# Performance work log

Hardware: AMD Instinct MI355X
Metric: run time of the kernel (lower is better)

## Reference

```python
import math
import jax, jax.numpy as jnp
import numpy as np

DMODEL = 512
NUM_HEADS = 8
HEAD_DIM = DMODEL // NUM_HEADS
MAX_LEN = 1024
L = 2 * MAX_LEN - 1  # 2047
B = 4
S = 1024  # src_len == max_len


def setup_inputs() -> dict:
    key = jax.random.key(0)
    ks = jax.random.split(key, 12)
    f32 = jnp.float32
    inp = {
        "query": jax.random.normal(ks[0], (B, S, DMODEL), f32),
        "key": jax.random.normal(ks[1], (B, S, DMODEL), f32),
        "value": jax.random.normal(ks[2], (B, S, DMODEL), f32),
        # nn.Linear weights (y = x @ W.T + b)
        "Wq": jax.random.normal(ks[3], (DMODEL, DMODEL), f32) * 0.02,
        "bq": jnp.zeros((DMODEL,), f32),
        "Wk": jax.random.normal(ks[4], (DMODEL, DMODEL), f32) * 0.02,
        "bk": jnp.zeros((DMODEL,), f32),
        "Wv": jax.random.normal(ks[5], (DMODEL, DMODEL), f32) * 0.02,
        "bv": jnp.zeros((DMODEL,), f32),
        # relative position tables (torch.randn init)
        "quaver_Er": jax.random.normal(ks[6], (NUM_HEADS, L, HEAD_DIM), f32),
        "beat_Er": jax.random.normal(ks[7], (NUM_HEADS, L // 4, HEAD_DIM), f32),
        "bar_Er": jax.random.normal(ks[8], (NUM_HEADS, L // 16, HEAD_DIM), f32),
    }
    return inp


def _skew(QEr):
    # QEr: [b, h, S, 2S-1] -> [b, h, S, S] via pad-reshape-slice trick
    b, h, s, l = QEr.shape
    x = jnp.pad(QEr, ((0, 0), (0, 0), (0, 0), (0, 1)))        # [b,h,S,2S]
    x = x.reshape(b, h, -1)                                    # [b,h,S*2S]
    x = jnp.pad(x, ((0, 0), (0, 0), (0, l - s)))               # [b,h,(S+1)*(2S-1)]
    x = x.reshape(b, h, s + 1, l)
    return x[:, :, :s, -s:]


def _skew_chunked(QEr, rep):
    # Faithful to skew_beat/skew_bar: repeat_interleave(rep) along last dim, then
    # roll each chunk of `rep` rows (chunk i) by i*rep, then take last S cols.
    b, h, s, lr = QEr.shape
    x = jnp.repeat(QEr, rep, axis=-1)                          # [b,h,S,rep*lr]
    w = rep * lr
    shifts = (jnp.arange(s) // rep) * rep                      # [S]
    # torch.roll: out[c] = in[(c - shift) mod W]
    cols = (jnp.arange(w)[None, :] - shifts[:, None]) % w      # [S, W]
    x = jnp.take_along_axis(x, cols[None, None], axis=-1)
    return x[:, :, :s, -s:]


def reference(query, key, value, Wq, bq, Wk, bk, Wv, bv, quaver_Er, beat_Er, bar_Er):
    bs, src_len, d_model = query.shape
    h, hd = NUM_HEADS, HEAD_DIM
    max_len = MAX_LEN

    q = (query @ Wq.T + bq).reshape(bs, src_len, h, hd).transpose(0, 2, 1, 3)   # [b,h,S,d]
    k = (key @ Wk.T + bk).reshape(bs, src_len, h, hd).transpose(0, 2, 3, 1)      # [b,h,d,S]
    v = (value @ Wv.T + bv).reshape(bs, src_len, h, hd).transpose(0, 2, 1, 3)    # [b,h,S,d]

    Er_q = quaver_Er[:, max_len - src_len:max_len + src_len, :]                  # [h,2S-1,d]
    Er_b = beat_Er[:, (max_len - src_len) // 4:(max_len + src_len) // 4, :]      # [h,~S/2,d]
    Er_r = bar_Er[:, (max_len - src_len) // 16:(max_len + src_len) // 16, :]     # [h,~S/8,d]

    QEr_q = jnp.einsum('bhsd,hld->bhsl', q, Er_q)
    QEr_b = jnp.einsum('bhsd,hld->bhsl', q, Er_b)
    QEr_r = jnp.einsum('bhsd,hld->bhsl', q, Er_r)

    Srel = _skew(QEr_q)
    Srel_beat = _skew_chunked(QEr_b, 4)
    Srel_bar = _skew_chunked(QEr_r, 16)

    attn = (jnp.matmul(q, k) + Srel + Srel_beat + Srel_bar) / math.sqrt(hd)
    attn = jax.nn.softmax(attn, axis=-1)
    out = jnp.matmul(attn, v)                                                    # [b,h,S,d]
    out = out.transpose(0, 2, 1, 3).reshape(bs, src_len, d_model)
    return out, attn
```

## Files before the change

kernel.cpp:

```cpp
#include <hip/hip_runtime.h>


typedef float f32x4 __attribute__((ext_vector_type(4)));
typedef short s16x8 __attribute__((ext_vector_type(8)));
typedef short s16x4 __attribute__((ext_vector_type(4)));
typedef __bf16 bf16x8 __attribute__((ext_vector_type(8)));

static __device__ __forceinline__ short f2bf(float f) {
    return __builtin_bit_cast(short, (__bf16)f);
}
static __device__ __forceinline__ float bf2f(short s) {
    union { unsigned u; float f; } v;
    v.u = ((unsigned)(unsigned short)s) << 16;
    return v.f;
}
static __device__ __forceinline__ f32x4 MM(s16x8 a, s16x8 b, f32x4 c) {
    return __builtin_amdgcn_mfma_f32_16x16x32_bf16(
        __builtin_bit_cast(bf16x8, a), __builtin_bit_cast(bf16x8, b), c, 0, 0, 0);
}
#define KEEP(x) asm volatile("" : "+v"(x))

struct CvtArgs {
    const float* src[9];
    short* dst[9];
    unsigned n[9];
};

__global__ __launch_bounds__(256) void convert_kernel(CvtArgs a) {
    const int ai = blockIdx.y;
    const unsigned n = a.n[ai];
    const float* __restrict__ s = a.src[ai];
    short* __restrict__ d = a.dst[ai];
    const unsigned stride = gridDim.x * 256 * 8;
    for (unsigned base = (blockIdx.x * 256 + threadIdx.x) * 8; base < n; base += stride) {
        f32x4 v0 = *(const f32x4*)(s + base);
        f32x4 v1 = *(const f32x4*)(s + base + 4);
        s16x8 o;
        o[0] = f2bf(v0[0]); o[1] = f2bf(v0[1]); o[2] = f2bf(v0[2]); o[3] = f2bf(v0[3]);
        o[4] = f2bf(v1[0]); o[5] = f2bf(v1[1]); o[6] = f2bf(v1[2]); o[7] = f2bf(v1[3]);
        *(s16x8*)(d + base) = o;
    }
}

__global__ __launch_bounds__(128, 2) void proj_kernel(
    const short* __restrict__ queryb, const short* __restrict__ keyb, const short* __restrict__ valueb,
    const short* __restrict__ Wqb, const float* __restrict__ bq,
    const short* __restrict__ Wkb, const float* __restrict__ bk,
    const short* __restrict__ Wvb, const float* __restrict__ bv,
    short* __restrict__ qb, short* __restrict__ kb, short* __restrict__ vT)
{
    const int tid = threadIdx.x;
    const int wid = tid >> 6, lane = tid & 63;
    const int l15 = lane & 15, grp = lane >> 4;
    const int gid = blockIdx.x * 2 + wid;
    const int z = gid >> 9;
    const int r = gid & 511;

    const short *Am, *Bm;
    const float* bias;
    int a0, b0;
    if (z == 0)      { Am = Wqb;    Bm = queryb; bias = bq; a0 = (r >> 6) * 64; b0 = (r & 63) * 64; }
    else if (z == 1) { Am = Wkb;    Bm = keyb;   bias = bk; a0 = (r >> 6) * 64; b0 = (r & 63) * 64; }
    else             { Am = valueb; Bm = Wvb;    bias = bv; a0 = (r >> 3) * 64; b0 = (r & 7) * 64; }

    f32x4 acc[4][4];
    #pragma unroll
    for (int i = 0; i < 4; ++i)
        #pragma unroll
        for (int j = 0; j < 4; ++j)
            acc[i][j] = f32x4{0.f, 0.f, 0.f, 0.f};

    const short* arow0 = Am + (size_t)(a0 + l15) * 512 + grp * 8;
    const short* brow0 = Bm + (size_t)(b0 + l15) * 512 + grp * 8;

    s16x8 aA[4], bA[4], aB[4], bB[4];
    #pragma unroll
    for (int i = 0; i < 4; ++i) {
        aA[i] = *(const s16x8*)(arow0 + (size_t)i * 16 * 512);
        bA[i] = *(const s16x8*)(brow0 + (size_t)i * 16 * 512);
    }
    for (int kk = 0; kk < 512; kk += 32) {
        const int kn = kk + 32;
        if (kn < 512) {
            #pragma unroll
            for (int i = 0; i < 4; ++i) {
                aB[i] = *(const s16x8*)(arow0 + (size_t)i * 16 * 512 + kn);
                bB[i] = *(const s16x8*)(brow0 + (size_t)i * 16 * 512 + kn);
            }
        }
        #pragma unroll
        for (int i = 0; i < 4; ++i)
            #pragma unroll
            for (int j = 0; j < 4; ++j)
                acc[i][j] = MM(aA[i], bA[j], acc[i][j]);
        #pragma unroll
        for (int i = 0; i < 4; ++i) { aA[i] = aB[i]; bA[i] = bB[i]; }
    }

    if (z < 2) {
        short* dst = (z == 0) ? qb : kb;
        #pragma unroll
        for (int i = 0; i < 4; ++i) {
            const int f0 = a0 + i * 16 + grp * 4;
            const f32x4 bv4 = *(const f32x4*)&bias[f0];
            const int h = f0 >> 6, d0 = f0 & 63;
            #pragma unroll
            for (int j = 0; j < 4; ++j) {
                const int srow = b0 + j * 16 + l15;
                const int bb = srow >> 10, sl = srow & 1023;
                s16x4 o;
                #pragma unroll
                for (int g = 0; g < 4; ++g)
                    o[g] = f2bf(acc[i][j][g] + bv4[g]);
                *(s16x4*)&dst[(size_t)((bb * 8 + h) * 1024 + sl) * 64 + d0] = o;
            }
        }
    } else {
        #pragma unroll
        for (int j = 0; j < 4; ++j) {
            const int n = b0 + j * 16 + l15;
            const float bval = bias[n];
            const int h = n >> 6, d = n & 63;
            #pragma unroll
            for (int i = 0; i < 4; ++i) {
                const int s0 = a0 + i * 16 + grp * 4;
                const int bb = s0 >> 10, sl = s0 & 1023;
                s16x4 o;
                #pragma unroll
                for (int g = 0; g < 4; ++g)
                    o[g] = f2bf(acc[i][j][g] + bval);
                *(s16x4*)&vT[(size_t)((bb * 8 + h) * 64 + d) * 1024 + sl] = o;
            }
        }
    }
}

__global__ __launch_bounds__(512, 2) void attn_kernel(
    const short* __restrict__ Eqb, const short* __restrict__ Ebb, const short* __restrict__ Errb,
    const short* __restrict__ qb, const short* __restrict__ kb, const short* __restrict__ vT,
    float* __restrict__ out, float* __restrict__ attn)
{
    __shared__ __align__(16) char smem[155008];
    short* PS   = (short*)(smem + 86784);
    float* PACC = (float*)(smem + 119680);

    const int tid = threadIdx.x;
    const int wid = tid >> 6, lane = tid & 63;
    const int l15 = lane & 15, grp = lane >> 4;

    const int orig = blockIdx.x;
    const int bid = (orig & 7) * 32 + (orig >> 3);

    const int bh = bid >> 3;
    const int chunk = bid & 7;
    const int h = bh & 7;
    const int b = bh >> 3;

    const short* EqH = Eqb  + (size_t)h * 2047 * 64;
    const short* EbH = Ebb  + (size_t)h * 511 * 64;
    const short* ErH = Errb + (size_t)h * 127 * 64;
    const short* qbH = qb + (size_t)bh * 1024 * 64;
    const short* kbH = kb + (size_t)bh * 1024 * 64;
    const short* vTH = vT + (size_t)bh * 64 * 1024;

    auto buildT = [&](int i0s, int bb01, s16x8 q0, s16x8 q1) {
        short* RQ2 = (short*)(smem + bb01 * 32896);
        short* RB2 = (short*)(smem + 65792 + bb01 * 8320);
        short* RR2 = (short*)(smem + 82432 + bb01 * 2176);
        const int qbase = 1008 - i0s;
        for (int cs = wid; cs < 65; cs += 8) {
            const int c = cs * 16 + l15;
            int erow = qbase + c; if (erow > 2046) erow = 2046;
            const short* ep = EqH + (size_t)erow * 64 + grp * 8;
            s16x8 e0 = *(const s16x8*)ep;
            s16x8 e1 = *(const s16x8*)(ep + 32);
            f32x4 a = f32x4{0.f, 0.f, 0.f, 0.f};
            a = MM(q0, e0, a);
            a = MM(q1, e1, a);
            #pragma unroll
            for (int g = 0; g < 4; ++g) {
                const int ii = grp * 4 + g;
                const int j = c - 15 + ii;
                if (j >= 0 && j < 1024) RQ2[ii * 1028 + j] = f2bf(a[g]);
            }
        }
        const int bbase = 252 - (i0s >> 2);
        for (int cs = wid; cs < 17; cs += 8) {
            const int c = cs * 16 + l15;
            int erow = bbase + c; if (erow > 510) erow = 510;
            const short* ep = EbH + (size_t)erow * 64 + grp * 8;
            s16x8 e0 = *(const s16x8*)ep;
            s16x8 e1 = *(const s16x8*)(ep + 32);
            f32x4 a = f32x4{0.f, 0.f, 0.f, 0.f};
            a = MM(q0, e0, a);
            a = MM(q1, e1, a);
            const int jq = c - 3 + grp;
            if (jq >= 0 && jq < 256) {
                #pragma unroll
                for (int g = 0; g < 4; ++g)
                    RB2[(grp * 4 + g) * 260 + jq] = f2bf(a[g]);
            }
        }
        const int rbase = 63 - (i0s >> 4);
        if (wid < 4) {
            const int c = wid * 16 + l15;
            const short* ep = ErH + (size_t)(rbase + c) * 64 + grp * 8;
            s16x8 e0 = *(const s16x8*)ep;
            s16x8 e1 = *(const s16x8*)(ep + 32);
            f32x4 a = f32x4{0.f, 0.f, 0.f, 0.f};
            a = MM(q0, e0, a);
            a = MM(q1, e1, a);
            #pragma unroll
            for (int g = 0; g < 4; ++g)
                RR2[(grp * 4 + g) * 68 + c] = f2bf(a[g]);
        }
    };

    const int i00 = chunk * 128;
    s16x8 qA0 = *(const s16x8*)(qbH + (size_t)(i00 + l15) * 64 + grp * 8);
    s16x8 qA1 = *(const s16x8*)(qbH + (size_t)(i00 + l15) * 64 + 32 + grp * 8);

    s16x8 kf[8][2];
    #pragma unroll
    for (int t = 0; t < 8; ++t) {
        const short* kp = kbH + (size_t)(wid * 128 + t * 16 + l15) * 64 + grp * 8;
        kf[t][0] = *(const s16x8*)kp;
        kf[t][1] = *(const s16x8*)(kp + 32);
    }
    s16x8 vreg[16];
    #pragma unroll
    for (int dvt = 0; dvt < 4; ++dvt)
        #pragma unroll
        for (int kc = 0; kc < 4; ++kc)
            vreg[dvt * 4 + kc] = *(const s16x8*)(vTH + (size_t)(dvt * 16 + l15) * 1024
                                                 + wid * 128 + kc * 32 + grp * 8);

    buildT(i00, 0, qA0, qA1);
    __syncthreads();

    const float SC = 0.125f * 1.4426950408889634f;
    const int swz = (l15 & 3) << 5;

    for (int s = 0; s < 8; ++s) {
        #pragma unroll
        for (int t = 0; t < 8; ++t) { KEEP(kf[t][0]); KEEP(kf[t][1]); }
        #pragma unroll
        for (int z = 0; z < 16; ++z) KEEP(vreg[z]);

        const int cur = s & 1;
        const int i0 = chunk * 128 + s * 16;
        short* RQ2c = (short*)(smem + cur * 32896);
        short* RB2c = (short*)(smem + 65792 + cur * 8320);
        short* RR2c = (short*)(smem + 82432 + cur * 2176);
        float* RSUMc = (float*)(smem + 154496 + cur * 256);

        s16x8 qn0, qn1;
        if (s < 7) {
            qn0 = *(const s16x8*)(qbH + (size_t)(i0 + 16 + l15) * 64 + grp * 8);
            qn1 = *(const s16x8*)(qbH + (size_t)(i0 + 16 + l15) * 64 + 32 + grp * 8);
        }

        f32x4 p[8];
        #pragma unroll
        for (int t = 0; t < 8; ++t) {
            f32x4 a = f32x4{0.f, 0.f, 0.f, 0.f};
            a = MM(kf[t][0], qA0, a);
            a = MM(kf[t][1], qA1, a);
            const int jb2 = wid * 128 + t * 16 + grp * 4;
            s16x4 gq4 = *(const s16x4*)&RQ2c[l15 * 1028 + jb2];
            const float rb = bf2f(RB2c[l15 * 260 + wid * 32 + t * 4 + grp]);
            const float rr = bf2f(RR2c[l15 * 68 + wid * 8 + t]);
            const float add = rb + rr;
            f32x4 pe;
            #pragma unroll
            for (int g = 0; g < 4; ++g)
                pe[g] = exp2f((a[g] + bf2f(gq4[g]) + add) * SC);
            p[t] = pe;
        }

        float part = 0.f;
        #pragma unroll
        for (int t = 0; t < 8; ++t)
            #pragma unroll
            for (int g = 0; g < 4; ++g)
                part += p[t][g];
        part += __shfl_xor(part, 16, 64);
        part += __shfl_xor(part, 32, 64);
        if (lane < 16) RSUMc[lane * 8 + wid] = part;

        #pragma unroll
        for (int t = 0; t < 8; ++t) {
            const int col = (wid * 128 + t * 16 + grp * 4) ^ swz;
            s16x4 o;
            #pragma unroll
            for (int g = 0; g < 4; ++g) o[g] = f2bf(p[t][g]);
            *(s16x4*)&PS[l15 * 1028 + col] = o;
        }
        __syncthreads();

        float rinv;
        {
            f32x4 s0 = *(const f32x4*)&RSUMc[l15 * 8];
            f32x4 s1 = *(const f32x4*)&RSUMc[l15 * 8 + 4];
            rinv = 1.0f / (s0[0] + s0[1] + s0[2] + s0[3] + s1[0] + s1[1] + s1[2] + s1[3]);
        }

        if (s < 7) buildT(i0 + 16, cur ^ 1, qn0, qn1);

        f32x4 acc[4];
        #pragma unroll
        for (int dvt = 0; dvt < 4; ++dvt) acc[dvt] = f32x4{0.f, 0.f, 0.f, 0.f};
        #pragma unroll
        for (int kc = 0; kc < 4; ++kc) {
            const int col = (wid * 128 + kc * 32 + grp * 8) ^ swz;
            s16x8 bfrag = *(const s16x8*)&PS[l15 * 1028 + col];
            #pragma unroll
            for (int dvt = 0; dvt < 4; ++dvt)
                acc[dvt] = MM(vreg[dvt * 4 + kc], bfrag, acc[dvt]);
        }
        #pragma unroll
        for (int dvt = 0; dvt < 4; ++dvt)
            *(f32x4*)&PACC[(wid * 16 + l15) * 68 + dvt * 16 + grp * 4] = acc[dvt];
        __syncthreads();

        if (tid < 256) {
            const int i = tid >> 4, dvq = tid & 15;
            f32x4 o = f32x4{0.f, 0.f, 0.f, 0.f};
            #pragma unroll
            for (int w = 0; w < 8; ++w)
                o += *(const f32x4*)&PACC[(w * 16 + i) * 68 + dvq * 4];
            f32x4 s0 = *(const f32x4*)&RSUMc[i * 8];
            f32x4 s1 = *(const f32x4*)&RSUMc[i * 8 + 4];
            const float ri = 1.0f / (s0[0] + s0[1] + s0[2] + s0[3] + s1[0] + s1[1] + s1[2] + s1[3]);
            o *= ri;
            *(f32x4*)&out[(size_t)(b * 1024 + i0 + i) * 512 + h * 64 + dvq * 4] = o;
        }

        {
            float* arow = attn + (size_t)(bh * 1024 + i0 + l15) * 1024;
            #pragma unroll
            for (int t = 0; t < 8; ++t) {
                f32x4 o = p[t] * rinv;
                *(f32x4*)&arow[wid * 128 + t * 16 + grp * 4] = o;
            }
        }

        if (s < 7) { qA0 = qn0; qA1 = qn1; }
    }
}

extern "C" void kernel_launch(void* const* d_in, const int* in_sizes, int n_in,
                              void* d_out, int out_size, void* d_ws, size_t ws_size,
                              hipStream_t stream)
{
    const float* query = (const float*)d_in[0];
    const float* key   = (const float*)d_in[1];
    const float* value = (const float*)d_in[2];
    const float* Wq = (const float*)d_in[3];
    const float* bq = (const float*)d_in[4];
    const float* Wk = (const float*)d_in[5];
    const float* bk = (const float*)d_in[6];
    const float* Wv = (const float*)d_in[7];
    const float* bv = (const float*)d_in[8];
    const float* Eq = (const float*)d_in[9];
    const float* Eb = (const float*)d_in[10];
    const float* Er = (const float*)d_in[11];

    float* out  = (float*)d_out;
    float* attn = out + (size_t)4 * 1024 * 512;

    short* qb     = (short*)d_ws;
    short* kb     = qb     + 2097152;
    short* vT     = kb     + 2097152;
    short* queryb = vT     + 2097152;
    short* keyb   = queryb + 2097152;
    short* valueb = keyb   + 2097152;
    short* Wqb    = valueb + 2097152;
    short* Wkb    = Wqb    + 262144;
    short* Wvb    = Wkb    + 262144;
    short* Eqb    = Wvb    + 262144;
    short* Ebb    = Eqb    + 1048064;
    short* Errb   = Ebb    + 261632;

    CvtArgs a;
    a.src[0] = query; a.dst[0] = queryb; a.n[0] = 2097152;
    a.src[1] = key;   a.dst[1] = keyb;   a.n[1] = 2097152;
    a.src[2] = value; a.dst[2] = valueb; a.n[2] = 2097152;
    a.src[3] = Wq;    a.dst[3] = Wqb;    a.n[3] = 262144;
    a.src[4] = Wk;    a.dst[4] = Wkb;    a.n[4] = 262144;
    a.src[5] = Wv;    a.dst[5] = Wvb;    a.n[5] = 262144;
    a.src[6] = Eq;    a.dst[6] = Eqb;    a.n[6] = 1048064;
    a.src[7] = Eb;    a.dst[7] = Ebb;    a.n[7] = 261632;
    a.src[8] = Er;    a.dst[8] = Errb;   a.n[8] = 65024;

    convert_kernel<<<dim3(1024, 9), 256, 0, stream>>>(a);
    proj_kernel<<<768, 128, 0, stream>>>(queryb, keyb, valueb,
                                         Wqb, bq, Wkb, bk, Wvb, bv, qb, kb, vT);
    attn_kernel<<<256, 512, 0, stream>>>(Eqb, Ebb, Errb, qb, kb, vT, out, attn);
}
```

Before: 129.5 us.

## Split fused attention into per-tile softmax and PV kernels with local rel-pos tables

Replaces the 256-block fused attention kernel, which looped over 8 row tiles and kept K and V in registers, with a 2048-block softmax kernel and a separate PV kernel. Each softmax block computes only the 16x128 slice of each relative-position table its wave needs, so shared memory drops and more blocks fit per CU. The PV kernel reads the normalized fp32 attention back from global memory and converts it to bf16. This aims for more parallelism and occupancy, but adds a full extra read of the 16MB attention matrix plus an extra launch. The convert kernel grid is also reduced.

New measurement: 185.6 us. 43.3% more time.

```diff
diff --git a/kernel.cpp b/kernel.cpp
--- a/kernel.cpp
+++ b/kernel.cpp
@@ -18,7 +18,6 @@
     return __builtin_amdgcn_mfma_f32_16x16x32_bf16(
         __builtin_bit_cast(bf16x8, a), __builtin_bit_cast(bf16x8, b), c, 0, 0, 0);
 }
-#define KEEP(x) asm volatile("" : "+v"(x))
 
 struct CvtArgs {
     const float* src[9];
@@ -135,42 +134,44 @@
     }
 }
 
-__global__ __launch_bounds__(512, 2) void attn_kernel(
+__global__ __launch_bounds__(512, 4) void softmax_kernel(
     const short* __restrict__ Eqb, const short* __restrict__ Ebb, const short* __restrict__ Errb,
-    const short* __restrict__ qb, const short* __restrict__ kb, const short* __restrict__ vT,
-    float* __restrict__ out, float* __restrict__ attn)
+    const short* __restrict__ qb, const short* __restrict__ kb,
+    float* __restrict__ attn)
 {
-    __shared__ __align__(16) char smem[155008];
-    short* PS   = (short*)(smem + 86784);
-    float* PACC = (float*)(smem + 119680);
+    __shared__ __align__(16) char smem[45568];
+    float* RSUM = (float*)(smem + 45056);
 
     const int tid = threadIdx.x;
     const int wid = tid >> 6, lane = tid & 63;
     const int l15 = lane & 15, grp = lane >> 4;
 
     const int orig = blockIdx.x;
-    const int bid = (orig & 7) * 32 + (orig >> 3);
-
-    const int bh = bid >> 3;
-    const int chunk = bid & 7;
+    const int bid = (orig & 7) * 256 + (orig >> 3);
+
+    const int bh = bid >> 6;
+    const int i0 = (bid & 63) << 4;
     const int h = bh & 7;
-    const int b = bh >> 3;
 
     const short* EqH = Eqb  + (size_t)h * 2047 * 64;
     const short* EbH = Ebb  + (size_t)h * 511 * 64;
     const short* ErH = Errb + (size_t)h * 127 * 64;
     const short* qbH = qb + (size_t)bh * 1024 * 64;
     const short* kbH = kb + (size_t)bh * 1024 * 64;
-    const short* vTH = vT + (size_t)bh * 64 * 1024;
-
-    auto buildT = [&](int i0s, int bb01, s16x8 q0, s16x8 q1) {
-        short* RQ2 = (short*)(smem + bb01 * 32896);
-        short* RB2 = (short*)(smem + 65792 + bb01 * 8320);
-        short* RR2 = (short*)(smem + 82432 + bb01 * 2176);
-        const int qbase = 1008 - i0s;
-        for (int cs = wid; cs < 65; cs += 8) {
-            const int c = cs * 16 + l15;
-            int erow = qbase + c; if (erow > 2046) erow = 2046;
+
+    short* LRQ = (short*)(smem + wid * 5632);
+    short* LRB = LRQ + 16 * 132;
+    short* LRR = LRB + 16 * 36;
+
+    s16x8 q0 = *(const s16x8*)(qbH + (size_t)(i0 + l15) * 64 + grp * 8);
+    s16x8 q1 = *(const s16x8*)(qbH + (size_t)(i0 + l15) * 64 + 32 + grp * 8);
+
+    {
+        const int E0 = 1023 - i0 + wid * 128 - 16;
+        #pragma unroll 2
+        for (int ck = 0; ck < 10; ++ck) {
+            int erow = E0 + ck * 16 + l15;
+            erow = erow < 0 ? 0 : (erow > 2046 ? 2046 : erow);
             const short* ep = EqH + (size_t)erow * 64 + grp * 8;
             s16x8 e0 = *(const s16x8*)ep;
             s16x8 e1 = *(const s16x8*)(ep + 32);
@@ -180,173 +181,145 @@
             #pragma unroll
             for (int g = 0; g < 4; ++g) {
                 const int ii = grp * 4 + g;
-                const int j = c - 15 + ii;
-                if (j >= 0 && j < 1024) RQ2[ii * 1028 + j] = f2bf(a[g]);
-            }
-        }
-        const int bbase = 252 - (i0s >> 2);
-        for (int cs = wid; cs < 17; cs += 8) {
-            const int c = cs * 16 + l15;
-            int erow = bbase + c; if (erow > 510) erow = 510;
+                const int jl = ck * 16 + l15 + ii - 16;
+                if (jl >= 0 && jl < 128) LRQ[ii * 132 + jl] = f2bf(a[g]);
+            }
+        }
+    }
+    {
+        const int B0 = 255 - (i0 >> 2) + wid * 32 - 4;
+        #pragma unroll
+        for (int ck = 0; ck < 3; ++ck) {
+            int erow = B0 + ck * 16 + l15;
+            erow = erow < 0 ? 0 : (erow > 510 ? 510 : erow);
             const short* ep = EbH + (size_t)erow * 64 + grp * 8;
             s16x8 e0 = *(const s16x8*)ep;
             s16x8 e1 = *(const s16x8*)(ep + 32);
             f32x4 a = f32x4{0.f, 0.f, 0.f, 0.f};
             a = MM(q0, e0, a);
             a = MM(q1, e1, a);
-            const int jq = c - 3 + grp;
-            if (jq >= 0 && jq < 256) {
-                #pragma unroll
-                for (int g = 0; g < 4; ++g)
-                    RB2[(grp * 4 + g) * 260 + jq] = f2bf(a[g]);
-            }
-        }
-        const int rbase = 63 - (i0s >> 4);
-        if (wid < 4) {
-            const int c = wid * 16 + l15;
-            const short* ep = ErH + (size_t)(rbase + c) * 64 + grp * 8;
-            s16x8 e0 = *(const s16x8*)ep;
-            s16x8 e1 = *(const s16x8*)(ep + 32);
-            f32x4 a = f32x4{0.f, 0.f, 0.f, 0.f};
-            a = MM(q0, e0, a);
-            a = MM(q1, e1, a);
+            #pragma unroll
+            for (int g = 0; g < 4; ++g) {
+                const int ii = grp * 4 + g;
+                const int jql = ck * 16 + l15 + (ii >> 2) - 4;
+                if (jql >= 0 && jql < 32) LRB[ii * 36 + jql] = f2bf(a[g]);
+            }
+        }
+    }
+    {
+        const int R0 = 63 - (i0 >> 4) + wid * 8;
+        int erow = R0 + l15;
+        erow = erow > 126 ? 126 : erow;
+        const short* ep = ErH + (size_t)erow * 64 + grp * 8;
+        s16x8 e0 = *(const s16x8*)ep;
+        s16x8 e1 = *(const s16x8*)(ep + 32);
+        f32x4 a = f32x4{0.f, 0.f, 0.f, 0.f};
+        a = MM(q0, e0, a);
+        a = MM(q1, e1, a);
+        if (l15 < 8) {
             #pragma unroll
             for (int g = 0; g < 4; ++g)
-                RR2[(grp * 4 + g) * 68 + c] = f2bf(a[g]);
-        }
-    };
-
-    const int i00 = chunk * 128;
-    s16x8 qA0 = *(const s16x8*)(qbH + (size_t)(i00 + l15) * 64 + grp * 8);
-    s16x8 qA1 = *(const s16x8*)(qbH + (size_t)(i00 + l15) * 64 + 32 + grp * 8);
-
-    s16x8 kf[8][2];
+                LRR[(grp * 4 + g) * 8 + l15] = f2bf(a[g]);
+        }
+    }
+
+    const float SC = 0.125f * 1.4426950408889634f;
+    f32x4 p[8];
+    float part = 0.f;
     #pragma unroll
     for (int t = 0; t < 8; ++t) {
-        const short* kp = kbH + (size_t)(wid * 128 + t * 16 + l15) * 64 + grp * 8;
-        kf[t][0] = *(const s16x8*)kp;
-        kf[t][1] = *(const s16x8*)(kp + 32);
-    }
-    s16x8 vreg[16];
+        const int jb = wid * 128 + t * 16;
+        const short* kp = kbH + (size_t)(jb + l15) * 64 + grp * 8;
+        s16x8 kf0 = *(const s16x8*)kp;
+        s16x8 kf1 = *(const s16x8*)(kp + 32);
+        f32x4 a = f32x4{0.f, 0.f, 0.f, 0.f};
+        a = MM(kf0, q0, a);
+        a = MM(kf1, q1, a);
+        s16x4 gq4 = *(const s16x4*)&LRQ[l15 * 132 + t * 16 + grp * 4];
+        const float rb = bf2f(LRB[l15 * 36 + t * 4 + grp]);
+        const float rr = bf2f(LRR[l15 * 8 + t]);
+        const float add = rb + rr;
+        f32x4 pe;
+        #pragma unroll
+        for (int g = 0; g < 4; ++g) {
+            pe[g] = __builtin_amdgcn_exp2f((a[g] + bf2f(gq4[g]) + add) * SC);
+            part += pe[g];
+        }
+        p[t] = pe;
+    }
+
+    part += __shfl_xor(part, 16, 64);
+    part += __shfl_xor(part, 32, 64);
+    if (lane < 16) RSUM[lane * 8 + wid] = part;
+    __syncthreads();
+
+    float rinv;
+    {
+        f32x4 s0 = *(const f32x4*)&RSUM[l15 * 8];
+        f32x4 s1 = *(const f32x4*)&RSUM[l15 * 8 + 4];
+        rinv = 1.0f / (s0[0] + s0[1] + s0[2] + s0[3] + s1[0] + s1[1] + s1[2] + s1[3]);
+    }
+
+    float* arow = attn + (size_t)(bh * 1024 + i0 + l15) * 1024;
+    #pragma unroll
+    for (int t = 0; t < 8; ++t) {
+        f32x4 o = p[t] * rinv;
+        *(f32x4*)&arow[wid * 128 + t * 16 + grp * 4] = o;
+    }
+}
+
+__global__ __launch_bounds__(256, 6) void pv_kernel(
+    const float* __restrict__ attn, const short* __restrict__ vT,
+    float* __restrict__ out)
+{
+    __shared__ __align__(16) float PACC[4 * 16 * 68];
+
+    const int tid = threadIdx.x;
+    const int wid = tid >> 6, lane = tid & 63;
+    const int l15 = lane & 15, grp = lane >> 4;
+
+    const int orig = blockIdx.x;
+    const int bid = (orig & 7) * 256 + (orig >> 3);
+
+    const int bh = bid >> 6;
+    const int i0 = (bid & 63) << 4;
+    const int h = bh & 7;
+    const int b = bh >> 3;
+
+    const float* aH = attn + (size_t)(bh * 1024 + i0 + l15) * 1024;
+    const short* vTH = vT + (size_t)bh * 64 * 1024;
+
+    const int c0 = wid * 256;
+    f32x4 acc[4];
+    #pragma unroll
+    for (int dvt = 0; dvt < 4; ++dvt) acc[dvt] = f32x4{0.f, 0.f, 0.f, 0.f};
+
+    #pragma unroll
+    for (int kc = 0; kc < 8; ++kc) {
+        const int col = c0 + kc * 32 + grp * 8;
+        f32x4 a0 = *(const f32x4*)&aH[col];
+        f32x4 a1 = *(const f32x4*)&aH[col + 4];
+        s16x8 pfrag;
+        #pragma unroll
+        for (int g = 0; g < 4; ++g) { pfrag[g] = f2bf(a0[g]); pfrag[4 + g] = f2bf(a1[g]); }
+        #pragma unroll
+        for (int dvt = 0; dvt < 4; ++dvt) {
+            s16x8 vfrag = *(const s16x8*)&vTH[(size_t)(dvt * 16 + l15) * 1024 + col];
+            acc[dvt] = MM(vfrag, pfrag, acc[dvt]);
+        }
+    }
+
     #pragma unroll
     for (int dvt = 0; dvt < 4; ++dvt)
-        #pragma unroll
-        for (int kc = 0; kc < 4; ++kc)
-            vreg[dvt * 4 + kc] = *(const s16x8*)(vTH + (size_t)(dvt * 16 + l15) * 1024
-                                                 + wid * 128 + kc * 32 + grp * 8);
-
-    buildT(i00, 0, qA0, qA1);
+        *(f32x4*)&PACC[(wid * 16 + l15) * 68 + dvt * 16 + grp * 4] = acc[dvt];
     __syncthreads();
 
-    const float SC = 0.125f * 1.4426950408889634f;
-    const int swz = (l15 & 3) << 5;
-
-    for (int s = 0; s < 8; ++s) {
-        #pragma unroll
-        for (int t = 0; t < 8; ++t) { KEEP(kf[t][0]); KEEP(kf[t][1]); }
-        #pragma unroll
-        for (int z = 0; z < 16; ++z) KEEP(vreg[z]);
-
-        const int cur = s & 1;
-        const int i0 = chunk * 128 + s * 16;
-        short* RQ2c = (short*)(smem + cur * 32896);
-        short* RB2c = (short*)(smem + 65792 + cur * 8320);
-        short* RR2c = (short*)(smem + 82432 + cur * 2176);
-        float* RSUMc = (float*)(smem + 154496 + cur * 256);
-
-        s16x8 qn0, qn1;
-        if (s < 7) {
-            qn0 = *(const s16x8*)(qbH + (size_t)(i0 + 16 + l15) * 64 + grp * 8);
-            qn1 = *(const s16x8*)(qbH + (size_t)(i0 + 16 + l15) * 64 + 32 + grp * 8);
-        }
-
-        f32x4 p[8];
-        #pragma unroll
-        for (int t = 0; t < 8; ++t) {
-            f32x4 a = f32x4{0.f, 0.f, 0.f, 0.f};
-            a = MM(kf[t][0], qA0, a);
-            a = MM(kf[t][1], qA1, a);
-            const int jb2 = wid * 128 + t * 16 + grp * 4;
-            s16x4 gq4 = *(const s16x4*)&RQ2c[l15 * 1028 + jb2];
-            const float rb = bf2f(RB2c[l15 * 260 + wid * 32 + t * 4 + grp]);
-            const float rr = bf2f(RR2c[l15 * 68 + wid * 8 + t]);
-            const float add = rb + rr;
-            f32x4 pe;
-            #pragma unroll
-            for (int g = 0; g < 4; ++g)
-                pe[g] = exp2f((a[g] + bf2f(gq4[g]) + add) * SC);
-            p[t] = pe;
-        }
-
-        float part = 0.f;
-        #pragma unroll
-        for (int t = 0; t < 8; ++t)
-            #pragma unroll
-            for (int g = 0; g < 4; ++g)
-                part += p[t][g];
-        part += __shfl_xor(part, 16, 64);
-        part += __shfl_xor(part, 32, 64);
-        if (lane < 16) RSUMc[lane * 8 + wid] = part;
-
-        #pragma unroll
-        for (int t = 0; t < 8; ++t) {
-            const int col = (wid * 128 + t * 16 + grp * 4) ^ swz;
-            s16x4 o;
-            #pragma unroll
-            for (int g = 0; g < 4; ++g) o[g] = f2bf(p[t][g]);
-            *(s16x4*)&PS[l15 * 1028 + col] = o;
-        }
-        __syncthreads();
-
-        float rinv;
-        {
-            f32x4 s0 = *(const f32x4*)&RSUMc[l15 * 8];
-            f32x4 s1 = *(const f32x4*)&RSUMc[l15 * 8 + 4];
-            rinv = 1.0f / (s0[0] + s0[1] + s0[2] + s0[3] + s1[0] + s1[1] + s1[2] + s1[3]);
-        }
-
-        if (s < 7) buildT(i0 + 16, cur ^ 1, qn0, qn1);
-
-        f32x4 acc[4];
-        #pragma unroll
-        for (int dvt = 0; dvt < 4; ++dvt) acc[dvt] = f32x4{0.f, 0.f, 0.f, 0.f};
-        #pragma unroll
-        for (int kc = 0; kc < 4; ++kc) {
-            const int col = (wid * 128 + kc * 32 + grp * 8) ^ swz;
-            s16x8 bfrag = *(const s16x8*)&PS[l15 * 1028 + col];
-            #pragma unroll
-            for (int dvt = 0; dvt < 4; ++dvt)
-                acc[dvt] = MM(vreg[dvt * 4 + kc], bfrag, acc[dvt]);
-        }
-        #pragma unroll
-        for (int dvt = 0; dvt < 4; ++dvt)
-            *(f32x4*)&PACC[(wid * 16 + l15) * 68 + dvt * 16 + grp * 4] = acc[dvt];
-        __syncthreads();
-
-        if (tid < 256) {
-            const int i = tid >> 4, dvq = tid & 15;
-            f32x4 o = f32x4{0.f, 0.f, 0.f, 0.f};
-            #pragma unroll
-            for (int w = 0; w < 8; ++w)
-                o += *(const f32x4*)&PACC[(w * 16 + i) * 68 + dvq * 4];
-            f32x4 s0 = *(const f32x4*)&RSUMc[i * 8];
-            f32x4 s1 = *(const f32x4*)&RSUMc[i * 8 + 4];
-            const float ri = 1.0f / (s0[0] + s0[1] + s0[2] + s0[3] + s1[0] + s1[1] + s1[2] + s1[3]);
-            o *= ri;
-            *(f32x4*)&out[(size_t)(b * 1024 + i0 + i) * 512 + h * 64 + dvq * 4] = o;
-        }
-
-        {
-            float* arow = attn + (size_t)(bh * 1024 + i0 + l15) * 1024;
-            #pragma unroll
-            for (int t = 0; t < 8; ++t) {
-                f32x4 o = p[t] * rinv;
-                *(f32x4*)&arow[wid * 128 + t * 16 + grp * 4] = o;
-            }
-        }
-
-        if (s < 7) { qA0 = qn0; qA1 = qn1; }
-    }
+    const int i = tid >> 4, dq = tid & 15;
+    f32x4 o = f32x4{0.f, 0.f, 0.f, 0.f};
+    #pragma unroll
+    for (int w = 0; w < 4; ++w)
+        o += *(const f32x4*)&PACC[(w * 16 + i) * 68 + dq * 4];
+    *(f32x4*)&out[(size_t)(b * 1024 + i0 + i) * 512 + h * 64 + dq * 4] = o;
 }
 
 extern "C" void kernel_launch(void* const* d_in, const int* in_sizes, int n_in,
@@ -393,8 +366,9 @@
     a.src[7] = Eb;    a.dst[7] = Ebb;    a.n[7] = 261632;
     a.src[8] = Er;    a.dst[8] = Errb;   a.n[8] = 65024;
 
-    convert_kernel<<<dim3(1024, 9), 256, 0, stream>>>(a);
+    convert_kernel<<<dim3(128, 9), 256, 0, stream>>>(a);
     proj_kernel<<<768, 128, 0, stream>>>(queryb, keyb, valueb,
                                          Wqb, bq, Wkb, bk, Wvb, bv, qb, kb, vT);
-    attn_kernel<<<256, 512, 0, stream>>>(Eqb, Ebb, Errb, qb, kb, vT, out, attn);
-}
+    softmax_kernel<<<2048, 512, 0, stream>>>(Eqb, Ebb, Errb, qb, kb, attn);
+    pv_kernel<<<2048, 256, 0, stream>>>(attn, vT, out);
+}
```
